# Kernel tuning notes

Hardware: AMD Instinct MI355X
Metric: run time of the kernel (lower is better)

## Reference

```python
import jax, jax.numpy as jnp
import numpy as np
import math

HID, H = 384, 4
D = HID // H  # 96, HGT head dim
N_T = [2048, 2048, 2048, 1024, 1024]  # user_turn, ai_turn, stance, pressure, belief
OFF = [0, 2048, 4096, 6144, 7168]
NTOT = 8192
# (src_type, dst_type, num_edges)
EDGES = [(0, 1, 32768), (1, 0, 32768), (1, 2, 32768), (2, 2, 32768),
         (0, 3, 16384), (3, 1, 32768), (1, 4, 16384), (4, 2, 32768)]
E_OFF = np.concatenate([[0], np.cumsum([c for _, _, c in EDGES])]).tolist()


def _gelu(x):
    return jax.nn.gelu(x, approximate=False)


def _ln(x, g, b, eps=1e-5):
    m = x.mean(-1, keepdims=True)
    v = ((x - m) ** 2).mean(-1, keepdims=True)
    return (x - m) * jax.lax.rsqrt(v + eps) * g + b


def _mha(q_in, kv_in, Wqkv, bqkv, Wo, bo):
    # torch nn.MultiheadAttention (batch_first, batch=1); Wqkv stored [E, 3E]
    E = HID
    q = (q_in @ Wqkv[:, :E] + bqkv[:E]).reshape(-1, H, D)
    k = (kv_in @ Wqkv[:, E:2 * E] + bqkv[E:2 * E]).reshape(-1, H, D)
    v = (kv_in @ Wqkv[:, 2 * E:] + bqkv[2 * E:]).reshape(-1, H, D)
    s = jnp.einsum('qhd,khd->hqk', q, k) / math.sqrt(D)
    w = jax.nn.softmax(s, axis=-1)
    o = jnp.einsum('hqk,khd->qhd', w, v).reshape(-1, E)
    return o @ Wo + bo


def _forward(x_user, x_ai, x_stance, x_pressure, x_belief,
             hgt_Wkqv, hgt_bkqv, hgt_Wout, hgt_bout, hgt_krel, hgt_vrel, hgt_prel, hgt_skip,
             ln_g, ln_b, sp_W, sp_b, sp_lng, sp_lnb, fc0_W, fc0_b, bn_g, bn_b,
             tq_W, tq_b, tk_W, tk_b, tv_W, tv_b, mha_Wqkv, mha_bqkv, mha_Wo, mha_bo,
             c1_W, c1_b, c2_W, c2_b, op_W, op_b, as1_W, as1_b, as2_W, as2_b,
             sc1_W, sc1_b, sc2_W, sc2_b, cl1_W, cl1_b, cl_lng, cl_lnb,
             cl2_W, cl2_b, cl3_W, cl3_b, tp_W, tp_b, edge_src, edge_dst):
    xs = [x_user, x_ai, x_stance, x_pressure, x_belief]
    for l in range(2):
        kqv = [x @ hgt_Wkqv[l, t] + hgt_bkqv[l, t] for t, x in enumerate(xs)]
        kk = [a[:, :HID].reshape(-1, H, D) for a in kqv]
        qq = [a[:, HID:2 * HID].reshape(-1, H, D) for a in kqv]
        vv = [a[:, 2 * HID:].reshape(-1, H, D) for a in kqv]
        al, msg, dgl = [], [], []
        for r, (s, d, cnt) in enumerate(EDGES):
            si = edge_src[E_OFF[r]:E_OFF[r + 1]]
            di = edge_dst[E_OFF[r]:E_OFF[r + 1]]
            ke = jnp.einsum('ehd,hdf->ehf', kk[s][si], hgt_krel[l, r])
            ve = jnp.einsum('ehd,hdf->ehf', vv[s][si], hgt_vrel[l, r])
            a = (qq[d][di] * ke).sum(-1) * hgt_prel[l, r] / math.sqrt(D)  # [E_r, H]
            al.append(a); msg.append(ve); dgl.append(di + OFF[d])
        a = jnp.concatenate(al); ve = jnp.concatenate(msg); dg = jnp.concatenate(dgl)
        mx = jax.ops.segment_max(a, dg, num_segments=NTOT)
        ex = jnp.exp(a - mx[dg])
        den = jax.ops.segment_sum(ex, dg, num_segments=NTOT)
        w = ex / den[dg]
        agg = jax.ops.segment_sum(ve * w[:, :, None], dg, num_segments=NTOT).reshape(NTOT, HID)
        new = []
        for t, x in enumerate(xs):
            o = _gelu(agg[OFF[t]:OFF[t] + N_T[t]]) @ hgt_Wout[l, t] + hgt_bout[l, t]
            g = jax.nn.sigmoid(hgt_skip[l, t])
            new.append(g * o + (1 - g) * x)
        xs = [_ln(_gelu(v), ln_g[t], ln_b[t]) for t, v in enumerate(new)]
    user_h, ai_h, stance_h, pressure_h, belief_h = xs

    # ---- StanceTrajectoryEncoder ----
    hs = _gelu(_ln(stance_h @ sp_W + sp_b, sp_lng, sp_lnb))

    def bn(x, i):  # eval-mode BatchNorm1d, running stats (0, 1)
        return x * (bn_g[i] / math.sqrt(1.0 + 1e-5)) + bn_b[i]

    xg = jax.nn.relu(bn(hs @ fc0_W + fc0_b, 0))
    Ns = hs.shape[0]
    for i in range(2):  # SGFormer TransConv layers (linear global attention)
        q = (xg @ tq_W[i] + tq_b[i]).reshape(Ns, H, HID)
        k = (xg @ tk_W[i] + tk_b[i]).reshape(Ns, H, HID)
        v = (xg @ tv_W[i] + tv_b[i]).reshape(Ns, H, HID)
        qn = q / jnp.linalg.norm(q)  # global Frobenius norm, as in SGFormer
        kn = k / jnp.linalg.norm(k)
        kvs = jnp.einsum('lhm,lhd->hmd', kn, v)
        num = jnp.einsum('nhm,hmd->nhd', qn, kvs) + Ns * v
        dnm = jnp.einsum('nhm,hm->nh', qn, kn.sum(0))[:, :, None] + Ns
        z = (num / dnm).mean(axis=1)  # mean over heads
        xg = jax.nn.relu(bn(0.5 * z + 0.5 * xg, i + 1))  # residual alpha=0.5
    h_mixed = 0.7 * hs + 0.3 * xg
    traj = _mha(h_mixed, h_mixed, mha_Wqkv[1], mha_bqkv[1], mha_Wo[1], mha_bo[1])
    traj_summary = traj.mean(0, keepdims=True)  # [1, HID]
    ci = h_mixed.T[None]  # [1, C, L]
    dn = ('NCH', 'OIH', 'NCH')
    c = jax.lax.conv_general_dilated(ci, c1_W, (1,), [(1, 1)], dimension_numbers=dn) + c1_b[None, :, None]
    c = _gelu(c)
    c = jax.lax.conv_general_dilated(c, c2_W, (1,), [(1, 1)], dimension_numbers=dn) + c2_b[None, :, None]
    c = _gelu(c)
    decay_summary = c.mean(axis=2)  # [1, HID//2]
    traj_emb = jnp.concatenate([traj_summary, decay_summary], -1) @ op_W + op_b

    # ---- PressureResponseModule ----
    ai_ctx = _mha(ai_h, user_h, mha_Wqkv[0], mha_bqkv[0], mha_Wo[0], mha_bo[0])
    ml = min(N_T[1], N_T[0])
    comb = jnp.concatenate([ai_h[:ml], user_h[:ml]], -1)
    pscores = jax.nn.sigmoid((jax.nn.relu(comb @ as1_W + as1_b) @ as2_W + as2_b)[:, 0])
    ai_pooled = ai_ctx.mean(0, keepdims=True)

    # ---- belief attention + stance comparison + classifier ----
    bctx = _mha(ai_h, belief_h, mha_Wqkv[2], mha_bqkv[2], mha_Wo[2], mha_bo[2]).mean(0, keepdims=True)
    sd_in = jnp.concatenate([stance_h[0:1], stance_h[-1:]], -1)
    stance_delta = jax.nn.relu(sd_in @ sc1_W + sc1_b) @ sc2_W + sc2_b
    comb2 = jnp.concatenate([traj_emb, ai_pooled, bctx, stance_delta], -1)  # [1, 1344]
    z = jax.nn.relu(_ln(comb2 @ cl1_W + cl1_b, cl_lng, cl_lnb))
    z = jax.nn.relu(z @ cl2_W + cl2_b)
    logits = (z @ cl3_W + cl3_b).reshape(())
    decay = jax.nn.sigmoid(logits)
    per_turn = jax.nn.sigmoid((ai_ctx @ tp_W + tp_b)[:, 0])
    return logits, decay, per_turn, pscores


def setup_inputs() -> dict:
    key = jax.random.key(0)
    ks = iter(jax.random.split(key, 128))

    def P(shape, fan_in):
        return jax.random.normal(next(ks), shape, jnp.float32) / np.float32(math.sqrt(fan_in))

    inp = {}
    for name, n in zip(['x_user', 'x_ai', 'x_stance', 'x_pressure', 'x_belief'], N_T):
        inp[name] = jax.random.normal(next(ks), (n, HID), jnp.float32)
    inp['hgt_Wkqv'] = P((2, 5, HID, 3 * HID), HID)
    inp['hgt_bkqv'] = jnp.zeros((2, 5, 3 * HID))
    inp['hgt_Wout'] = P((2, 5, HID, HID), HID)
    inp['hgt_bout'] = jnp.zeros((2, 5, HID))
    inp['hgt_krel'] = P((2, 8, H, D, D), D)
    inp['hgt_vrel'] = P((2, 8, H, D, D), D)
    inp['hgt_prel'] = jnp.ones((2, 8, H))
    inp['hgt_skip'] = jnp.ones((2, 5))
    inp['ln_g'] = jnp.ones((5, HID)); inp['ln_b'] = jnp.zeros((5, HID))
    inp['sp_W'] = P((HID, HID), HID); inp['sp_b'] = jnp.zeros((HID,))
    inp['sp_lng'] = jnp.ones((HID,)); inp['sp_lnb'] = jnp.zeros((HID,))
    inp['fc0_W'] = P((HID, HID), HID); inp['fc0_b'] = jnp.zeros((HID,))
    inp['bn_g'] = jnp.ones((3, HID)); inp['bn_b'] = jnp.zeros((3, HID))
    for nm in ['tq', 'tk', 'tv']:
        inp[nm + '_W'] = P((2, HID, H * HID), HID)
        inp[nm + '_b'] = jnp.zeros((2, H * HID))
    inp['mha_Wqkv'] = P((3, HID, 3 * HID), HID)
    inp['mha_bqkv'] = jnp.zeros((3, 3 * HID))
    inp['mha_Wo'] = P((3, HID, HID), HID)
    inp['mha_bo'] = jnp.zeros((3, HID))
    inp['c1_W'] = P((HID, HID, 3), HID * 3); inp['c1_b'] = jnp.zeros((HID,))
    inp['c2_W'] = P((HID // 2, HID, 3), HID * 3); inp['c2_b'] = jnp.zeros((HID // 2,))
    inp['op_W'] = P((HID + HID // 2, HID), HID + HID // 2); inp['op_b'] = jnp.zeros((HID,))
    inp['as1_W'] = P((2 * HID, HID), 2 * HID); inp['as1_b'] = jnp.zeros((HID,))
    inp['as2_W'] = P((HID, 1), HID); inp['as2_b'] = jnp.zeros((1,))
    inp['sc1_W'] = P((2 * HID, HID), 2 * HID); inp['sc1_b'] = jnp.zeros((HID,))
    inp['sc2_W'] = P((HID, HID // 2), HID); inp['sc2_b'] = jnp.zeros((HID // 2,))
    CIN = 3 * HID + HID // 2
    inp['cl1_W'] = P((CIN, HID), CIN); inp['cl1_b'] = jnp.zeros((HID,))
    inp['cl_lng'] = jnp.ones((HID,)); inp['cl_lnb'] = jnp.zeros((HID,))
    inp['cl2_W'] = P((HID, HID // 2), HID); inp['cl2_b'] = jnp.zeros((HID // 2,))
    inp['cl3_W'] = P((HID // 2, 1), HID // 2); inp['cl3_b'] = jnp.zeros((1,))
    inp['tp_W'] = P((HID, 1), HID); inp['tp_b'] = jnp.zeros((1,))
    srcs, dsts = [], []
    for (s, d, cnt) in EDGES:
        srcs.append(jax.random.randint(next(ks), (cnt,), 0, N_T[s], jnp.int32))
        dsts.append(jax.random.randint(next(ks), (cnt,), 0, N_T[d], jnp.int32))
    inp['edge_src'] = jnp.concatenate(srcs)
    inp['edge_dst'] = jnp.concatenate(dsts)
    return inp


def reference(x_user, x_ai, x_stance, x_pressure, x_belief,
              hgt_Wkqv, hgt_bkqv, hgt_Wout, hgt_bout, hgt_krel, hgt_vrel, hgt_prel, hgt_skip,
              ln_g, ln_b, sp_W, sp_b, sp_lng, sp_lnb, fc0_W, fc0_b, bn_g, bn_b,
              tq_W, tq_b, tk_W, tk_b, tv_W, tv_b, mha_Wqkv, mha_bqkv, mha_Wo, mha_bo,
              c1_W, c1_b, c2_W, c2_b, op_W, op_b, as1_W, as1_b, as2_W, as2_b,
              sc1_W, sc1_b, sc2_W, sc2_b, cl1_W, cl1_b, cl_lng, cl_lnb,
              cl2_W, cl2_b, cl3_W, cl3_b, tp_W, tp_b, edge_src, edge_dst):
    return _forward(x_user, x_ai, x_stance, x_pressure, x_belief,
                    hgt_Wkqv, hgt_bkqv, hgt_Wout, hgt_bout, hgt_krel, hgt_vrel, hgt_prel, hgt_skip,
                    ln_g, ln_b, sp_W, sp_b, sp_lng, sp_lnb, fc0_W, fc0_b, bn_g, bn_b,
                    tq_W, tq_b, tk_W, tk_b, tv_W, tv_b, mha_Wqkv, mha_bqkv, mha_Wo, mha_bo,
                    c1_W, c1_b, c2_W, c2_b, op_W, op_b, as1_W, as1_b, as2_W, as2_b,
                    sc1_W, sc1_b, sc2_W, sc2_b, cl1_W, cl1_b, cl_lng, cl_lnb,
                    cl2_W, cl2_b, cl3_W, cl3_b, tp_W, tp_b, edge_src, edge_dst)
```

## Files before the change

kernel.cpp:

```cpp
#include <hip/hip_runtime.h>
#include <hip/hip_bf16.h>

#define NEDGE 229376
#define NTOT  8192
#define BNCONST 0.9999950000374997f
#define ISQ96   0.10206207261596575f

__constant__ int c_NT[5]     = {2048,2048,2048,1024,1024};
__constant__ int c_OFFS[5]   = {0,2048,4096,6144,7168};
__constant__ int c_ESRC[8]   = {0,1,1,2,0,3,1,4};
__constant__ int c_EDST[8]   = {1,0,2,2,3,1,4,2};
__constant__ int c_EOFF[9]   = {0,32768,65536,98304,131072,147456,180224,196608,229376};
__constant__ int c_RELROW[8] = {0,2048,4096,6144,8192,10240,11264,13312};

static const int h_NT[5]   = {2048,2048,2048,1024,1024};
static const int h_OFFS[5] = {0,2048,4096,6144,7168};

__device__ inline float gelu_f(float x){ return 0.5f*x*(1.0f+erff(x*0.70710678118654752f)); }
__device__ inline float sigm(float x){ return 1.0f/(1.0f+expf(-x)); }
__device__ inline float wsum64(float v){
  #pragma unroll
  for (int s=32;s>0;s>>=1) v += __shfl_xor(v, s, 64);
  return v;
}
// ... 153 lines not shown
      float v = acc[i][j];
      if (bias) v += bias[gn];
      float s = kmul;
      if (cs) s *= cs[gn];
      v *= s;
      if (csh) v += csh[gn];
      if (act==1) v = fmaxf(v, 0.f);
      else if (act==2) v = gelu_f(v);
      C[(size_t)gm*ldc + gn] = v;
    }
  }
}

__global__ __launch_bounds__(256) void gemm128(
    const float* __restrict__ A, int lda, int sAz,
    const float* __restrict__ B, int ldb, int sBz,
    const float* __restrict__ bias, int sbz,
    float* __restrict__ C, int ldc, int sCz,
    int M, int N, int K, int act, int agelu, int tsel,
    const float* __restrict__ Bp1, const float* __restrict__ Bp2,
    const float* __restrict__ biasp1, const float* __restrict__ biasp2)
{
  __shared__ float As[16][68];
  __shared__ float Bs[16][132];
  int tid = threadIdx.x;
  int tx = tid & 15, ty = tid >> 4;
  int am = tid >> 2, ak = (tid & 3) * 4;
  int bk = tid >> 4, bn = (tid & 15) * 4;

  int nxy = gridDim.x * gridDim.y;
  int orig = blockIdx.y * gridDim.x + blockIdx.x;
  int q = nxy >> 3, r = nxy & 7;
  int xcd = orig & 7, rest = orig >> 3;
  int wg = ((xcd < r) ? xcd*(q+1) : r*(q+1) + (xcd - r)*q) + rest;
  int bx = wg % gridDim.x, by = wg / gridDim.x;
  int m0 = by * 64, n0 = bx * 128;

  int z = blockIdx.z;
  const float* Ab = A + (size_t)z * sAz;
  const float* Bb;
  const float* bb;
  if (Bp1){
    Bb = (z == 0) ? B : ((z == 1) ? Bp1 : Bp2);
    bb = (z == 0) ? bias : ((z == 1) ? biasp1 : biasp2);
  } else {
    Bb = B + (size_t)z * sBz;
    bb = bias ? (bias + (size_t)z * sbz) : nullptr;
  }
  float* Cb = C + (size_t)z * sCz;
  if (tsel){
    int t = row_type(m0);
    Bb = B + (size_t)t * sBz;
    bb = bias ? (bias + (size_t)t * sbz) : nullptr;
  }
  int gmA = m0 + am, gnB = n0 + bn;
  int ntiles = K >> 4;
  float4 ra, rb0, rb1;
  float acc[4][8] = {};

  auto fetch = [&](int kk){
    if (gmA < M){
      ra = *reinterpret_cast<const float4*>(&Ab[(size_t)gmA*lda + kk + ak]);
      if (agelu){
        ra.x=gelu_f(ra.x); ra.y=gelu_f(ra.y); ra.z=gelu_f(ra.z); ra.w=gelu_f(ra.w);
      }
    } else {
      ra = make_float4(0.f,0.f,0.f,0.f);
    }
    if (gnB + 67 < N){
      rb0 = *reinterpret_cast<const float4*>(&Bb[(size_t)(kk + bk)*ldb + gnB]);
      rb1 = *reinterpret_cast<const float4*>(&Bb[(size_t)(kk + bk)*ldb + gnB + 64]);
    } else {
      const float* bp = &Bb[(size_t)(kk + bk)*ldb];
      rb0.x = (gnB    < N) ? bp[gnB   ] : 0.f;
      rb0.y = (gnB+1  < N) ? bp[gnB+ 1] : 0.f;
      rb0.z = (gnB+2  < N) ? bp[gnB+ 2] : 0.f;
      rb0.w = (gnB+3  < N) ? bp[gnB+ 3] : 0.f;
      rb1.x = (gnB+64 < N) ? bp[gnB+64] : 0.f;
      rb1.y = (gnB+65 < N) ? bp[gnB+65] : 0.f;
      rb1.z = (gnB+66 < N) ? bp[gnB+66] : 0.f;
      rb1.w = (gnB+67 < N) ? bp[gnB+67] : 0.f;
    }
  };
  auto stage = [&](){
    As[ak  ][am] = ra.x;
    As[ak+1][am] = ra.y;
    As[ak+2][am] = ra.z;
    As[ak+3][am] = ra.w;
    *reinterpret_cast<float4*>(&Bs[bk][bn     ]) = rb0;
    *reinterpret_cast<float4*>(&Bs[bk][bn + 64]) = rb1;
  };

  fetch(0);
  for (int t = 0; t < ntiles; t++){
    if (t > 0) __syncthreads();
    stage();
    __syncthreads();
    if (t + 1 < ntiles) fetch((t+1) << 4);
    #pragma unroll
    for (int k = 0; k < 16; k++) {
      float4 a4 = *reinterpret_cast<const float4*>(&As[k][ty*4]);
      float4 b0 = *reinterpret_cast<const float4*>(&Bs[k][tx*4]);
      float4 b1 = *reinterpret_cast<const float4*>(&Bs[k][64 + tx*4]);
      float a[4] = {a4.x,a4.y,a4.z,a4.w};
      float b[8] = {b0.x,b0.y,b0.z,b0.w,b1.x,b1.y,b1.z,b1.w};
      #pragma unroll
      for (int i=0;i<4;i++)
        #pragma unroll
        for (int j=0;j<8;j++) acc[i][j] += a[i]*b[j];
    }
  }

  bool fullN = (n0 + 127 < N);
  int cb0 = n0 + tx*4, cb1 = n0 + 64 + tx*4;
  #pragma unroll
  for (int i=0;i<4;i++){
    int gm = m0 + ty*4 + i;
    if (gm >= M) continue;
    float v[8];
    #pragma unroll
    for (int jh=0; jh<2; jh++){
      #pragma unroll
      for (int j=0;j<4;j++){
        float x = acc[i][jh*4+j];
        int gn = (jh ? cb1 : cb0) + j;
        if (bb && gn < N) x += bb[gn];
        if (act==1) x = fmaxf(x, 0.f);
        else if (act==2) x = gelu_f(x);
        v[jh*4+j] = x;
      }
    }
    if (fullN){
      *reinterpret_cast<float4*>(&Cb[(size_t)gm*ldc + cb0]) = make_float4(v[0],v[1],v[2],v[3]);
      *reinterpret_cast<float4*>(&Cb[(size_t)gm*ldc + cb1]) = make_float4(v[4],v[5],v[6],v[7]);
    } else {
      #pragma unroll
      for (int jh=0; jh<2; jh++){
        #pragma unroll
        for (int j=0;j<4;j++){
          int gn = (jh ? cb1 : cb0) + j;
          if (gn < N) Cb[(size_t)gm*ldc + gn] = v[jh*4+j];
        }
      }
    }
  }
}

__global__ __launch_bounds__(256) void gemm_rel(
    const float* __restrict__ KQV_, const float* __restrict__ krel_l,
    const float* __restrict__ vrel_l, float* __restrict__ KE_, float* __restrict__ VE_)
{
  int z = blockIdx.z;
  int w = z & 1, h = (z >> 1) & 3, r = z >> 3;
  int s = c_ESRC[r];
  int Ns = c_NT[s];
  int m0 = blockIdx.y * 64;
  if (m0 >= Ns) return;
  int n0 = blockIdx.x * 64;
  const float* A = KQV_ + (size_t)c_OFFS[s]*1152 + (w ? 768 : 0) + h*96;
  const float* B = (w ? vrel_l : krel_l) + (size_t)(r*4 + h)*9216;
  float* C = (w ? VE_ : KE_) + (size_t)c_RELROW[r]*384 + h*96;

  __shared__ float As[2][16][68];
  __shared__ float Bs[2][16][68];
  int tid = threadIdx.x;
  int tx = tid & 15, ty = tid >> 4;
  int am = tid >> 2, ak = (tid & 3) * 4;
  int bk = tid >> 4, bn = (tid & 15) * 4;
  int gmA = m0 + am;
  int gnB = n0 + bn;
  float4 ra, rb;
  float acc[4][4] = {};

  auto fetch = [&](int kk){
    ra = (gmA < Ns) ? *reinterpret_cast<const float4*>(&A[(size_t)gmA*1152 + kk + ak])
                    : make_float4(0.f,0.f,0.f,0.f);
    if (gnB + 3 < 96){
      rb = *reinterpret_cast<const float4*>(&B[(size_t)(kk + bk)*96 + gnB]);
    } else {
      rb.x = (gnB   < 96) ? B[(size_t)(kk + bk)*96 + gnB  ] : 0.f;
      rb.y = (gnB+1 < 96) ? B[(size_t)(kk + bk)*96 + gnB+1] : 0.f;
      rb.z = (gnB+2 < 96) ? B[(size_t)(kk + bk)*96 + gnB+2] : 0.f;
      rb.w = (gnB+3 < 96) ? B[(size_t)(kk + bk)*96 + gnB+3] : 0.f;
    }
  };
  auto stage = [&](int b){
    As[b][ak  ][am] = ra.x;
    As[b][ak+1][am] = ra.y;
    As[b][ak+2][am] = ra.z;
    As[b][ak+3][am] = ra.w;
    *reinterpret_cast<float4*>(&Bs[b][bk][bn]) = rb;
  };

  fetch(0);
  stage(0);
  __syncthreads();
  for (int t = 0; t < 6; t++){
    int cur = t & 1;
    if (t + 1 < 6) fetch((t+1) << 4);
    #pragma unroll
    for (int k = 0; k < 16; k++) {
      float4 a4 = *reinterpret_cast<const float4*>(&As[cur][k][ty*4]);
      float4 b4 = *reinterpret_cast<const float4*>(&Bs[cur][k][tx*4]);
      float a[4] = {a4.x, a4.y, a4.z, a4.w};
      float b[4] = {b4.x, b4.y, b4.z, b4.w};
      #pragma unroll
      for (int i=0;i<4;i++)
        #pragma unroll
        for (int j=0;j<4;j++) acc[i][j] += a[i]*b[j];
    }
    if (t + 1 < 6) stage(cur ^ 1);
    __syncthreads();
  }
  #pragma unroll
  for (int i=0;i<4;i++){
    int gm = m0 + ty*4 + i; if (gm >= Ns) continue;
    #pragma unroll
    for (int j=0;j<4;j++){
      int gn = n0 + tx*4 + j; if (gn >= 96) continue;
      C[(size_t)gm*384 + gn] = acc[i][j];
    }
  }
}

__global__ __launch_bounds__(256) void gemm_atb_ks(
    const float* __restrict__ A0, int lda, const float* __restrict__ B0, int ldb,
    float* __restrict__ C0, int ldc, int M, int N, int L,
    int hsA, int hsB, int hsC, int nch)
{
  __shared__ float As[2][16][68];
  __shared__ float Bs[2][16][68];
  int h = blockIdx.z / nch, c = blockIdx.z % nch;
  const float* A = A0 + (size_t)h*hsA;
  const float* B = B0 + (size_t)h*hsB;
  float* C = C0 + (size_t)h*hsC;
  int l0 = c*256;
  int tid = threadIdx.x;
  int tx = tid & 15, ty = tid >> 4;
  int sl = tid >> 4, sq = (tid & 15) * 4;
  int m0 = blockIdx.y * 64, n0 = blockIdx.x * 64;
  int gmA = m0 + sq, gnB = n0 + sq;
  int ntiles = 16;
  float4 ra, rb;
  float acc[4][4] = {};

  auto fetch = [&](int ll){
    if (gmA + 3 < M){
      ra = *reinterpret_cast<const float4*>(&A[(size_t)(ll + sl)*lda + gmA]);
    } else {
      ra.x = (gmA   < M) ? A[(size_t)(ll + sl)*lda + gmA  ] : 0.f;
      ra.y = (gmA+1 < M) ? A[(size_t)(ll + sl)*lda + gmA+1] : 0.f;
      ra.z = (gmA+2 < M) ? A[(size_t)(ll + sl)*lda + gmA+2] : 0.f;
      ra.w = (gmA+3 < M) ? A[(size_t)(ll + sl)*lda + gmA+3] : 0.f;
    }
    if (gnB + 3 < N){
      rb = *reinterpret_cast<const float4*>(&B[(size_t)(ll + sl)*ldb + gnB]);
    } else {
      rb.x = (gnB   < N) ? B[(size_t)(ll + sl)*ldb + gnB  ] : 0.f;
      rb.y = (gnB+1 < N) ? B[(size_t)(ll + sl)*ldb + gnB+1] : 0.f;
      rb.z = (gnB+2 < N) ? B[(size_t)(ll + sl)*ldb + gnB+2] : 0.f;
      rb.w = (gnB+3 < N) ? B[(size_t)(ll + sl)*ldb + gnB+3] : 0.f;
    }
  };
  auto stage = [&](int b){
    *reinterpret_cast<float4*>(&As[b][sl][sq]) = ra;
    *reinterpret_cast<float4*>(&Bs[b][sl][sq]) = rb;
  };

  fetch(l0);
  stage(0);
  __syncthreads();
  for (int t = 0; t < ntiles; t++){
    int cur = t & 1;
    if (t + 1 < ntiles) fetch(l0 + ((t+1) << 4));
    #pragma unroll
    for (int l = 0; l < 16; l++) {
      float4 a4 = *reinterpret_cast<const float4*>(&As[cur][l][ty*4]);
      float4 b4 = *reinterpret_cast<const float4*>(&Bs[cur][l][tx*4]);
      float a[4] = {a4.x, a4.y, a4.z, a4.w};
      float b[4] = {b4.x, b4.y, b4.z, b4.w};
      #pragma unroll
      for (int i=0;i<4;i++)
        #pragma unroll
        for (int j=0;j<4;j++) acc[i][j] += a[i]*b[j];
    }
    if (t + 1 < ntiles) stage(cur ^ 1);
    __syncthreads();
  }
  #pragma unroll
  for (int i=0;i<4;i++){
    int gm = m0 + ty*4 + i; if (gm >= M) continue;
    #pragma unroll
    for (int j=0;j<4;j++){
      int gn = n0 + tx*4 + j; if (gn >= N) continue;
      atomicAdd(&C[(size_t)gm*ldc + gn], acc[i][j]);
    }
  }
}

__global__ __launch_bounds__(256) void fa_kernel(
    const float* __restrict__ MQ, int nq, float* __restrict__ OP, float* __restrict__ ML)
{
  __shared__ float Qs[96][68];
  __shared__ float Ksf[96][36];
  __shared__ float Vs[32][104];
  __shared__ float Ps[64][36];
  int tid = threadIdx.x;
  int tx = tid & 15, ty = tid >> 4;
  int q0 = blockIdx.x * 64;
  int h = blockIdx.y;
  int z = blockIdx.z, nch = gridDim.z;
  int kvbase = z * 512;

  #pragma unroll
  for (int i = 0; i < 6; i++){
    int e = tid + i*256;
    int r = e & 63, kq = (e >> 6) * 4;
    float4 f = *reinterpret_cast<const float4*>(&MQ[(size_t)(q0+r)*1152 + h*96 + kq]);
    Qs[kq  ][r] = f.x;
    Qs[kq+1][r] = f.y;
    Qs[kq+2][r] = f.z;
    Qs[kq+3][r] = f.w;
  }

  float m_i[4], l_i[4], acc[4][6];
  #pragma unroll
  for (int i=0;i<4;i++){
    m_i[i] = -3.0e38f; l_i[i] = 0.f;
    #pragma unroll
    for (int c=0;c<6;c++) acc[i][c] = 0.f;
  }
  int c0 = tx*6;
  __syncthreads();

  for (int t = 0; t < 16; t++){
    int kv0 = kvbase + t*32;
    #pragma unroll
    for (int i = 0; i < 3; i++){
      int e = tid + i*256;
      int n = e & 31, kq = (e >> 5) * 4;
      float4 f = *reinterpret_cast<const float4*>(&MQ[(size_t)(kv0+n)*1152 + 384 + h*96 + kq]);
      Ksf[kq  ][n] = f.x;
      Ksf[kq+1][n] = f.y;
      Ksf[kq+2][n] = f.z;
      Ksf[kq+3][n] = f.w;
      int nv = e / 24, cq = (e - nv*24) * 4;
      float4 g = *reinterpret_cast<const float4*>(&MQ[(size_t)(kv0+nv)*1152 + 768 + h*96 + cq]);
      *reinterpret_cast<float4*>(&Vs[nv][cq]) = g;
    }
    __syncthreads();

    float s0[4] = {0,0,0,0}, s1[4] = {0,0,0,0};
    #pragma unroll 8
    for (int k = 0; k < 96; k++){
      float4 a4 = *reinterpret_cast<const float4*>(&Qs[k][ty*4]);
      float2 b2 = *reinterpret_cast<const float2*>(&Ksf[k][tx*2]);
      s0[0] += a4.x*b2.x; s1[0] += a4.x*b2.y;
      s0[1] += a4.y*b2.x; s1[1] += a4.y*b2.y;
      s0[2] += a4.z*b2.x; s1[2] += a4.z*b2.y;
      s0[3] += a4.w*b2.x; s1[3] += a4.w*b2.y;
    }
    #pragma unroll
    for (int i=0;i<4;i++){
      float a = s0[i]*ISQ96, b = s1[i]*ISQ96;
      float rm = rgmax(fmaxf(a, b));
      float mn = fmaxf(m_i[i], rm);
      float alpha = expf(m_i[i] - mn);
      float p0 = expf(a - mn), p1 = expf(b - mn);
      float rs = rgsum(p0 + p1);
      l_i[i] = l_i[i]*alpha + rs;
      m_i[i] = mn;
      #pragma unroll
      for (int c=0;c<6;c++) acc[i][c] *= alpha;
      Ps[ty*4+i][tx*2  ] = p0;
      Ps[ty*4+i][tx*2+1] = p1;
    }
    __syncthreads();
    for (int kv = 0; kv < 32; kv++){
      float2 v01 = *reinterpret_cast<const float2*>(&Vs[kv][c0]);
      float2 v23 = *reinterpret_cast<const float2*>(&Vs[kv][c0+2]);
      float2 v45 = *reinterpret_cast<const float2*>(&Vs[kv][c0+4]);
      #pragma unroll
      for (int i=0;i<4;i++){
        float p = Ps[ty*4+i][kv];
        acc[i][0] += p*v01.x; acc[i][1] += p*v01.y;
        acc[i][2] += p*v23.x; acc[i][3] += p*v23.y;
        acc[i][4] += p*v45.x; acc[i][5] += p*v45.y;
      }
    }
    __syncthreads();
  }

  size_t base = ((size_t)(h*nch + z)*nq + q0);
  #pragma unroll
  for (int i=0;i<4;i++){
    size_t row = base + ty*4 + i;
    #pragma unroll
    for (int c=0;c<6;c++) OP[row*96 + c0 + c] = acc[i][c];
    if (tx == 0){
      ML[row*2  ] = m_i[i];
      ML[row*2+1] = l_i[i];
    }
  }
}

__global__ void k_famerge(const float* __restrict__ OP, const float* __restrict__ ML,
                          float* __restrict__ AO_, int nq, int nch){
  int e = blockIdx.x*256 + threadIdx.x;
  int total = 4*nq*96;
  if (e >= total) return;
  int c = e % 96;
  int q = (e / 96) % nq;
  int h = e / (96*nq);
  float M = -3.0e38f;
  for (int z = 0; z < nch; z++)
    M = fmaxf(M, ML[((size_t)(h*nch+z)*nq + q)*2]);
  float L = 0.f, O = 0.f;
  for (int z = 0; z < nch; z++){
    size_t row = (size_t)(h*nch+z)*nq + q;
    float w = expf(ML[row*2] - M);
    L += ML[row*2+1]*w;
    O += OP[row*96 + c]*w;
  }
  AO_[(size_t)q*384 + h*96 + c] = O / L;
}

__global__ void k_im2col(const float* __restrict__ in, float* __restrict__ imc){
  int e = blockIdx.x*256 + threadIdx.x;
  if (e >= 2048*1152) return;
  int p = e / 1152, k = e - p*1152;
  int ic = k / 3, j = k - ic*3;
  int gp = p - 1 + j;
  imc[e] = (gp >= 0 && gp < 2048) ? in[(size_t)gp*384 + ic] : 0.f;
}
__global__ void k_wtr(const float* __restrict__ W, float* __restrict__ WT, int OC){
  int e = blockIdx.x*256 + threadIdx.x;
  if (e >= OC*1152) return;
  int oc = e / 1152, k = e - oc*1152;
  WT[(size_t)k*OC + oc] = W[e];
}


__global__ __launch_bounds__(256) void k_escore(
    const float* __restrict__ KQV_, const float* __restrict__ KE_,
    const int* __restrict__ edg, const int* __restrict__ esr, const int* __restrict__ erl,
    const float* __restrict__ prel_l, float* __restrict__ EA)
{
  int e = blockIdx.x*4 + (threadIdx.x>>6);
  if (e >= NEDGE) return;
  int lane = threadIdx.x & 63;
  int h = lane >> 4, j = lane & 15;
  int dg = edg[e], sr = esr[e], r = erl[e];
  const float* q  = KQV_ + (size_t)dg*1152 + 384 + h*96;
  const float* ke = KE_  + (size_t)sr*384 + h*96;
  float p = 0.f;
  #pragma unroll
  for (int t=0;t<6;t++){ int d = j + t*16; p += q[d]*ke[d]; }
  p += __shfl_xor(p, 1, 64);
  p += __shfl_xor(p, 2, 64);
  p += __shfl_xor(p, 4, 64);
  p += __shfl_xor(p, 8, 64);
  if (j == 0) EA[(size_t)e*4 + h] = p * prel_l[r*4+h] * ISQ96;
}

__global__ void k_segmax(const float* __restrict__ EA, const int* __restrict__ edg,
                         unsigned* __restrict__ EMX){
  int i = blockIdx.x*256 + threadIdx.x;
  if (i >= NEDGE*4) return;
  int e = i >> 2, h = i & 3;
  atomicMax(&EMX[edg[e]*4 + h], encf(EA[i]));
}

__global__ void k_expsum(float* __restrict__ EA, const int* __restrict__ edg,
                         const unsigned* __restrict__ EMX, float* __restrict__ EDEN){
  int i = blockIdx.x*256 + threadIdx.x;
  if (i >= NEDGE*4) return;
  int e = i >> 2, h = i & 3;
  int dg = edg[e];
  float m = decf(EMX[dg*4 + h]);
  float ex = expf(EA[i] - m);
  EA[i] = ex;
  atomicAdd(&EDEN[dg*4 + h], ex);
}

__global__ __launch_bounds__(128) void k_agg(
    const float* __restrict__ EA, const float* __restrict__ VE_,
    const float* __restrict__ EDEN, const int* __restrict__ csr,
    const int* __restrict__ off, const int* __restrict__ esr, float* __restrict__ AGG)
{
  int node = blockIdx.x, tid = threadIdx.x;
  int b = off[node], e1 = off[node+1];
  int d0 = tid, d1 = tid+128, d2 = tid+256;
  int h0 = d0/96, h1 = d1/96, h2 = d2/96;
  float a0=0.f, a1=0.f, a2=0.f;
  if (e1 > b){
    float i0 = 1.0f/EDEN[node*4+h0];
    float i1 = 1.0f/EDEN[node*4+h1];
    float i2 = 1.0f/EDEN[node*4+h2];
    for (int p=b; p<e1; p++){
      int e = csr[p];
      const float* ve = VE_ + (size_t)esr[e]*384;
      const float* ea = EA + (size_t)e*4;
      a0 += ea[h0]*i0*ve[d0];
      a1 += ea[h1]*i1*ve[d1];
      a2 += ea[h2]*i2*ve[d2];
    }
  }
  AGG[(size_t)node*384 + d0] = a0;
  AGG[(size_t)node*384 + d1] = a1;
  AGG[(size_t)node*384 + d2] = a2;
}


__global__ __launch_bounds__(128) void k_gateln(
    const float* __restrict__ O, float* __restrict__ X,
    const float* __restrict__ skip_l, const float* __restrict__ lng, const float* __restrict__ lnb)
{
  __shared__ float red[2];
  int row = blockIdx.x, tid = threadIdx.x;
  int t = row_type(row);
  float gt = sigm(skip_l[t]);
  const float* o = O + (size_t)row*384;
  float* x = X + (size_t)row*384;
  float v0 = gelu_f(gt*o[tid]     + (1.f-gt)*x[tid]);
  float v1 = gelu_f(gt*o[tid+128] + (1.f-gt)*x[tid+128]);
  float v2 = gelu_f(gt*o[tid+256] + (1.f-gt)*x[tid+256]);
  int lane = tid & 63, wid = tid >> 6;
  float s = wsum64(v0+v1+v2);
  if (lane==0) red[wid] = s;
  __syncthreads();
  float mean = (red[0]+red[1]) * (1.0f/384.0f);
  __syncthreads();
  float d0=v0-mean, d1=v1-mean, d2=v2-mean;
  float q = wsum64(d0*d0+d1*d1+d2*d2);
  if (lane==0) red[wid] = q;
  __syncthreads();
  float var = (red[0]+red[1]) * (1.0f/384.0f);
  float rs = 1.0f/sqrtf(var + 1e-5f);
  const float* g = lng + (size_t)t*384;
  const float* b = lnb + (size_t)t*384;
  x[tid]     = d0*rs*g[tid]     + b[tid];
  x[tid+128] = d1*rs*g[tid+128] + b[tid+128];
  x[tid+256] = d2*rs*g[tid+256] + b[tid+256];
}

__global__ __launch_bounds__(128) void k_lnrow(
    const float* __restrict__ X, float* __restrict__ Y,
    const float* __restrict__ g, const float* __restrict__ b, int act)
{
  __shared__ float red[2];
  int row = blockIdx.x, tid = threadIdx.x;
  const float* x = X + (size_t)row*384;
  float* y = Y + (size_t)row*384;
  float v0 = x[tid], v1 = x[tid+128], v2 = x[tid+256];
  int lane = tid & 63, wid = tid >> 6;
  float s = wsum64(v0+v1+v2);
  if (lane==0) red[wid] = s;
  __syncthreads();
  float mean = (red[0]+red[1]) * (1.0f/384.0f);
  __syncthreads();
  float d0=v0-mean, d1=v1-mean, d2=v2-mean;
  float q = wsum64(d0*d0+d1*d1+d2*d2);
  if (lane==0) red[wid] = q;
  __syncthreads();
  float var = (red[0]+red[1]) * (1.0f/384.0f);
  float rs = 1.0f/sqrtf(var + 1e-5f);
  float u0 = d0*rs*g[tid]     + b[tid];
  float u1 = d1*rs*g[tid+128] + b[tid+128];
  float u2 = d2*rs*g[tid+256] + b[tid+256];
  if (act==1){ u0=fmaxf(u0,0.f); u1=fmaxf(u1,0.f); u2=fmaxf(u2,0.f); }
  else       { u0=gelu_f(u0); u1=gelu_f(u1); u2=gelu_f(u2); }
  y[tid] = u0; y[tid+128] = u1; y[tid+256] = u2;
}


__global__ __launch_bounds__(256) void k_sumsq(const float* __restrict__ x, int n, float* out){
  __shared__ float red[4];
  float s = 0.f;
  for (int i = blockIdx.x*256 + threadIdx.x; i < n; i += gridDim.x*256){ float v=x[i]; s += v*v; }
  s = wsum64(s);
  int lane = threadIdx.x & 63, wid = threadIdx.x >> 6;
  if (lane==0) red[wid] = s;
  __syncthreads();
  if (threadIdx.x==0) atomicAdd(out, red[0]+red[1]+red[2]+red[3]);
}

__global__ void k_colsum(const float* __restrict__ A, int R, int C, float scale,
                         float* __restrict__ out){
  int col = blockIdx.x*256 + threadIdx.x;
  if (col >= C) return;
  int nchunk = gridDim.y;
  int chunk = (R + nchunk - 1)/nchunk;
  int r0 = blockIdx.y*chunk, r1 = min(R, r0+chunk);
  float s = 0.f;
  for (int r=r0; r<r1; r++) s += A[(size_t)r*C + col];
  atomicAdd(&out[col], s*scale);
}

__global__ __launch_bounds__(256) void k_dnm(const float* __restrict__ QB,
    const float* __restrict__ KSUM, const float* __restrict__ sqsk, float* __restrict__ DNM){
  int wv = blockIdx.x*4 + (threadIdx.x>>6);
  int n = wv >> 2, h = wv & 3;
  int lane = threadIdx.x & 63;
  const float* q = QB + (size_t)n*1536 + h*384;
  const float* ks = KSUM + h*384;
  float p = 0.f;
  #pragma unroll
  for (int d=lane; d<384; d+=64) p += q[d]*ks[d];
  p = wsum64(p);
  if (lane==0) DNM[n*4+h] = p * (1.0f/sqrtf(sqsk[0]*sqsk[1])) + 2048.0f;
}

__global__ void k_zcomb(const float* __restrict__ ZN, const float* __restrict__ VB_,
                        const float* __restrict__ DNM_, const float* __restrict__ sqsk,
                        float* __restrict__ XG_,
                        const float* __restrict__ bng, const float* __restrict__ bnb){
  int i = blockIdx.x*256 + threadIdx.x;
  if (i >= 2048*384) return;
  int n = i / 384, c = i - n*384;
  float inv_s = 1.0f/sqrtf(sqsk[0]*sqsk[1]);
  float zm = 0.f;
  #pragma unroll
  for (int h=0;h<4;h++){
    float num = ZN[(size_t)n*1536 + h*384 + c]*inv_s + 2048.0f*VB_[(size_t)n*1536 + h*384 + c];
    zm += num / DNM_[n*4+h];
  }
  zm *= 0.25f;
  float y = 0.5f*zm + 0.5f*XG_[i];
  y = y * (bng[c] * BNCONST) + bnb[c];
  XG_[i] = fmaxf(y, 0.f);
}


__global__ __launch_bounds__(256) void k_gemv_ks(
    const float* __restrict__ in, int K, const float* __restrict__ W, int ldw,
    float* __restrict__ tmp, int N)
{
  int c = blockIdx.x*64 + (threadIdx.x & 63);
  int w = threadIdx.x >> 6;
  int kch = blockIdx.y, nk = gridDim.y;
  int k0 = (int)(((long long)K * kch) / nk);
  int k1 = (int)(((long long)K * (kch+1)) / nk);
  float s = 0.f;
  if (c < N){
    for (int k = k0 + w; k < k1; k += 4)
      s += in[k] * W[(size_t)k*ldw + c];
  }
  __shared__ float red[4][64];
  red[w][threadIdx.x & 63] = s;
  __syncthreads();
  if (w == 0 && c < N){
    int l = threadIdx.x & 63;
    tmp[(size_t)kch*N + c] = red[0][l] + red[1][l] + red[2][l] + red[3][l];
  }
}

__global__ void k_gemv_fin(const float* __restrict__ tmp, int nk,
                           const float* __restrict__ b, float* __restrict__ out, int N, int act){
  int c = blockIdx.x*256 + threadIdx.x;
  if (c >= N) return;
  float v = 0.f;
  for (int i = 0; i < nk; i++) v += tmp[(size_t)i*N + c];
  v += b[c];
  if (act==1) v = fmaxf(v, 0.f);
  out[c] = v;
}

__global__ __launch_bounds__(256) void k_rowdot(const float* __restrict__ A, int lda, int K,
    const float* __restrict__ w, const float* __restrict__ b, float* __restrict__ out, int M){
  int r = blockIdx.x*4 + (threadIdx.x>>6);
  if (r >= M) return;
  int lane = threadIdx.x & 63;
  const float* a = A + (size_t)r*lda;
  float p = 0.f;
  for (int k = lane; k < K; k += 64) p += a[k]*w[k];
  p = wsum64(p);
  if (lane==0) out[r] = sigm(p + b[0]);
}

__global__ __launch_bounds__(64) void k_final(const float* __restrict__ z2,
    const float* __restrict__ w, const float* __restrict__ b, float* __restrict__ out){
  int lane = threadIdx.x;
  float p = 0.f;
  for (int k = lane; k < 192; k += 64) p += z2[k]*w[k];
  p = wsum64(p);
  if (lane==0){
    float l = p + b[0];
    out[0] = l;
    out[1] = sigm(l);
  }
}


// ... 246 lines not shown
```

Baseline: 2.952 ms.

## Widen flash-attention KV tile to 64 and reuse K buffer for P

The flash-attention kernel now processes 64 keys per iteration instead of 32, so each thread computes a 4x4 score block and the online-softmax rescaling runs half as often. The K shared buffer is reused to hold the probability tile, and V is loaded in two 32-row halves to keep shared memory small. This is meant to raise arithmetic intensity in the QK^T loop and cut per-tile softmax and reduction overhead. In exchange it adds extra barriers and a serialized second V load inside each iteration, which may reduce overlap.

Measured after the change: 3.007 ms. Within noise of the previous version (+1.9%).

```diff
diff --git a/kernel.cpp b/kernel.cpp
--- a/kernel.cpp
+++ b/kernel.cpp
@@ -479,9 +479,8 @@
     const float* __restrict__ MQ, int nq, float* __restrict__ OP, float* __restrict__ ML)
 {
   __shared__ float Qs[96][68];
-  __shared__ float Ksf[96][36];
-  __shared__ float Vs[32][104];
-  __shared__ float Ps[64][36];
+  __shared__ float KP[96][68];
+  __shared__ float Vs[32][100];
   int tid = threadIdx.x;
   int tx = tid & 15, ty = tid >> 4;
   int q0 = blockIdx.x * 64;
@@ -508,49 +507,84 @@
     for (int c=0;c<6;c++) acc[i][c] = 0.f;
   }
   int c0 = tx*6;
-  __syncthreads();
-
-  for (int t = 0; t < 16; t++){
-    int kv0 = kvbase + t*32;
+
+  for (int t = 0; t < 8; t++){
+    int kv0 = kvbase + t*64;
+    __syncthreads();
+
+    #pragma unroll
+    for (int i = 0; i < 6; i++){
+      int e = tid + i*256;
+      int n = e & 63, kq = (e >> 6) * 4;
+      float4 f = *reinterpret_cast<const float4*>(&MQ[(size_t)(kv0+n)*1152 + 384 + h*96 + kq]);
+      KP[kq  ][n] = f.x;
+      KP[kq+1][n] = f.y;
+      KP[kq+2][n] = f.z;
+      KP[kq+3][n] = f.w;
+    }
     #pragma unroll
     for (int i = 0; i < 3; i++){
       int e = tid + i*256;
-      int n = e & 31, kq = (e >> 5) * 4;
-      float4 f = *reinterpret_cast<const float4*>(&MQ[(size_t)(kv0+n)*1152 + 384 + h*96 + kq]);
-      Ksf[kq  ][n] = f.x;
-      Ksf[kq+1][n] = f.y;
-      Ksf[kq+2][n] = f.z;
-      Ksf[kq+3][n] = f.w;
       int nv = e / 24, cq = (e - nv*24) * 4;
       float4 g = *reinterpret_cast<const float4*>(&MQ[(size_t)(kv0+nv)*1152 + 768 + h*96 + cq]);
       *reinterpret_cast<float4*>(&Vs[nv][cq]) = g;
     }
     __syncthreads();
 
-    float s0[4] = {0,0,0,0}, s1[4] = {0,0,0,0};
+    float s[4][4] = {};
     #pragma unroll 8
     for (int k = 0; k < 96; k++){
       float4 a4 = *reinterpret_cast<const float4*>(&Qs[k][ty*4]);
-      float2 b2 = *reinterpret_cast<const float2*>(&Ksf[k][tx*2]);
-      s0[0] += a4.x*b2.x; s1[0] += a4.x*b2.y;
-      s0[1] += a4.y*b2.x; s1[1] += a4.y*b2.y;
-      s0[2] += a4.z*b2.x; s1[2] += a4.z*b2.y;
-      s0[3] += a4.w*b2.x; s1[3] += a4.w*b2.y;
-    }
+      float4 b4 = *reinterpret_cast<const float4*>(&KP[k][tx*4]);
+      float a[4] = {a4.x, a4.y, a4.z, a4.w};
+      float b[4] = {b4.x, b4.y, b4.z, b4.w};
+      #pragma unroll
+      for (int i=0;i<4;i++)
+        #pragma unroll
+        for (int j=0;j<4;j++) s[i][j] += a[i]*b[j];
+    }
+    float p[4][4];
     #pragma unroll
     for (int i=0;i<4;i++){
-      float a = s0[i]*ISQ96, b = s1[i]*ISQ96;
-      float rm = rgmax(fmaxf(a, b));
+      float v0 = s[i][0]*ISQ96, v1 = s[i][1]*ISQ96;
+      float v2 = s[i][2]*ISQ96, v3 = s[i][3]*ISQ96;
+      float rm = rgmax(fmaxf(fmaxf(v0, v1), fmaxf(v2, v3)));
       float mn = fmaxf(m_i[i], rm);
       float alpha = expf(m_i[i] - mn);
-      float p0 = expf(a - mn), p1 = expf(b - mn);
-      float rs = rgsum(p0 + p1);
+      p[i][0] = expf(v0 - mn); p[i][1] = expf(v1 - mn);
+      p[i][2] = expf(v2 - mn); p[i][3] = expf(v3 - mn);
+      float rs = rgsum(p[i][0] + p[i][1] + p[i][2] + p[i][3]);
       l_i[i] = l_i[i]*alpha + rs;
       m_i[i] = mn;
       #pragma unroll
       for (int c=0;c<6;c++) acc[i][c] *= alpha;
-      Ps[ty*4+i][tx*2  ] = p0;
-      Ps[ty*4+i][tx*2+1] = p1;
+    }
+    __syncthreads();
+    #pragma unroll
+    for (int i=0;i<4;i++)
+      *reinterpret_cast<float4*>(&KP[ty*4+i][tx*4]) =
+          make_float4(p[i][0], p[i][1], p[i][2], p[i][3]);
+    __syncthreads();
+
+    for (int kv = 0; kv < 32; kv++){
+      float2 v01 = *reinterpret_cast<const float2*>(&Vs[kv][c0]);
+      float2 v23 = *reinterpret_cast<const float2*>(&Vs[kv][c0+2]);
+      float2 v45 = *reinterpret_cast<const float2*>(&Vs[kv][c0+4]);
+      #pragma unroll
+      for (int i=0;i<4;i++){
+        float pv = KP[ty*4+i][kv];
+        acc[i][0] += pv*v01.x; acc[i][1] += pv*v01.y;
+        acc[i][2] += pv*v23.x; acc[i][3] += pv*v23.y;
+        acc[i][4] += pv*v45.x; acc[i][5] += pv*v45.y;
+      }
+    }
+    __syncthreads();
+    #pragma unroll
+    for (int i = 0; i < 3; i++){
+      int e = tid + i*256;
+      int nv = e / 24, cq = (e - nv*24) * 4;
+      float4 g = *reinterpret_cast<const float4*>(&MQ[(size_t)(kv0+32+nv)*1152 + 768 + h*96 + cq]);
+      *reinterpret_cast<float4*>(&Vs[nv][cq]) = g;
     }
     __syncthreads();
     for (int kv = 0; kv < 32; kv++){
@@ -559,13 +593,12 @@
       float2 v45 = *reinterpret_cast<const float2*>(&Vs[kv][c0+4]);
       #pragma unroll
       for (int i=0;i<4;i++){
-        float p = Ps[ty*4+i][kv];
-        acc[i][0] += p*v01.x; acc[i][1] += p*v01.y;
-        acc[i][2] += p*v23.x; acc[i][3] += p*v23.y;
-        acc[i][4] += p*v45.x; acc[i][5] += p*v45.y;
+        float pv = KP[ty*4+i][32+kv];
+        acc[i][0] += pv*v01.x; acc[i][1] += pv*v01.y;
+        acc[i][2] += pv*v23.x; acc[i][3] += pv*v23.y;
+        acc[i][4] += pv*v45.x; acc[i][5] += pv*v45.y;
       }
     }
-    __syncthreads();
   }
 
   size_t base = ((size_t)(h*nch + z)*nq + q0);
```
